# Kernel tuning notes

Measured on AMD Instinct MI355X. Metric: run time of the kernel, lower is better.

## Reference

```python
import jax, jax.numpy as jnp
import numpy as np

N = 100000
E = 800000
D = 128


def setup_inputs() -> dict:
    key = jax.random.key(0)
    k1, k2, k3, k4 = jax.random.split(key, 4)
    x = jax.random.normal(k1, (N, D), dtype=jnp.float32)
    edge_index = jax.random.randint(k2, (2, E), 0, N, dtype=jnp.int64)
    s = 1.0 / np.sqrt(D)
    W1 = jax.random.uniform(k3, (D, D), jnp.float32, -s, s)
    b1 = jnp.zeros((D,), jnp.float32)
    W2 = jax.random.uniform(k4, (D, D), jnp.float32, -s, s)
    b2 = jnp.zeros((D,), jnp.float32)
    return {"x": x, "edge_index": edge_index, "W1": W1, "b1": b1, "W2": W2, "b2": b2}


def _degree(idx, n, dtype):
    return jax.ops.segment_sum(jnp.ones(idx.shape, dtype), idx, num_segments=n)


def _graph_conv(x, row, col, W, b, residual, act):
    n = x.shape[0]
    deg_out = jnp.clip(_degree(row, n, x.dtype), 1.0)          # [N]
    x_src = x * jax.lax.rsqrt(deg_out)[:, None]                # [N, D]
    # scatter-add messages from source (row) into target (col)
    agg = jax.ops.segment_sum(x_src[row], col, num_segments=n)  # [N, D]
    out = agg @ W.T + b
    deg_in = jnp.clip(_degree(col, n, x.dtype), 1.0)
    out = out * jax.lax.rsqrt(deg_in)[:, None]
    if residual:
        out = out + x  # res_fc is Identity (in_dim == out_dim)
    if act:
        out = jax.nn.relu(out)
    return out


def reference(x, edge_index, W1, b1, W2, b2):
    row, col = edge_index[0], edge_index[1]
    # layer 1: relu + residual; layer 2 (last, encoding=False): no act, no residual
    h = _graph_conv(x, row, col, W1, b1, residual=True, act=True)
    h = _graph_conv(h, row, col, W2, b2, residual=False, act=False)
    return h
```

## Files before the change

kernel.cpp:

```cpp
#include <hip/hip_runtime.h>


#define NN 100000
#define EE 800000
#define DD 128
#define NB1 98
#define NTILE (NN / 16)

typedef __attribute__((ext_vector_type(8))) short short8;
typedef __attribute__((ext_vector_type(4))) float floatx4;

__device__ inline float bf2f(unsigned int u16) {
    union { unsigned int i; float f; } c;
    c.i = u16 << 16;
    return c.f;
}
__device__ inline ushort f2bf(float f) {
    union { float f; unsigned int i; } c;
    c.f = f;
    unsigned int u = c.i;
    return (ushort)((u + 0x7fffu + ((u >> 16) & 1u)) >> 16);
}

__global__ __launch_bounds__(256) void count_kernel(const int* __restrict__ row,
                                                    const int* __restrict__ col,
                                                    int* __restrict__ cnt_out,
                                                    int* __restrict__ cnt_in,
                                                    int* __restrict__ off) {
    int e = blockIdx.x * 256 + threadIdx.x;
    if (e < EE) {
        off[e] = atomicAdd(&cnt_in[col[e]], 1);
        atomicAdd(&cnt_out[row[e]], 1);
    }
}

__global__ __launch_bounds__(256) void dinv_kernel(const int* __restrict__ cnt_out,
                                                   const int* __restrict__ cnt_in,
                                                   float* __restrict__ dinv_out,
                                                   float* __restrict__ dinv_in) {
    int n = blockIdx.x * 256 + threadIdx.x;
    if (n < NN) {
        dinv_out[n] = rsqrtf((float)max(cnt_out[n], 1));
        dinv_in[n]  = rsqrtf((float)max(cnt_in[n], 1));
    }
}

__global__ __launch_bounds__(256) void scan1_kernel(const int* __restrict__ cnt,
                                                    int* __restrict__ excl,
                                                    int* __restrict__ bsums) {
    __shared__ int tmp[256];
    const int t = threadIdx.x;
    const int base = blockIdx.x * 1024 + t * 4;
    int a[4];
#pragma unroll
    for (int q = 0; q < 4; ++q) a[q] = (base + q < NN) ? cnt[base + q] : 0;
    int s = a[0] + a[1] + a[2] + a[3];
    tmp[t] = s;
    __syncthreads();
    for (int off = 1; off < 256; off <<= 1) {
        int v = 0;
        if (t >= off) v = tmp[t - off];
        __syncthreads();
        tmp[t] += v;
        __syncthreads();
    }
    int excl_s = tmp[t] - s;
    if (t == 255) bsums[blockIdx.x] = tmp[t];
    int run = excl_s;
#pragma unroll
    for (int q = 0; q < 4; ++q) {
        if (base + q < NN) excl[base + q] = run;
        run += a[q];
    }
}

__global__ __launch_bounds__(256) void scan2_kernel(int* __restrict__ bsums, int nb) {
    __shared__ int tmp[256];
    const int t = threadIdx.x;
    int s = (t < nb) ? bsums[t] : 0;
    tmp[t] = s;
    __syncthreads();
    for (int off = 1; off < 256; off <<= 1) {
        int v = 0;
        if (t >= off) v = tmp[t - off];
        __syncthreads();
        tmp[t] += v;
        __syncthreads();
    }
    if (t < nb) bsums[t] = tmp[t] - s;
}

__global__ __launch_bounds__(256) void scan3_kernel(const int* __restrict__ excl,
                                                    const int* __restrict__ bsums,
                                                    int* __restrict__ row_start) {
    int i = blockIdx.x * 256 + threadIdx.x;
    if (i < NN) row_start[i] = excl[i] + bsums[i >> 10];
}

__global__ __launch_bounds__(256) void fill_kernel(const int* __restrict__ row,
                                                   const int* __restrict__ col,
                                                   const int* __restrict__ row_start,
                                                   const int* __restrict__ off,
                                                   int* __restrict__ srcs) {
    int e = blockIdx.x * 256 + threadIdx.x;
    if (e < EE) srcs[row_start[col[e]] + off[e]] = row[e];
}

__global__ __launch_bounds__(256) void prescale_kernel(const float* __restrict__ x,
                                                       const float* __restrict__ dinv_out,
                                                       ushort* __restrict__ xb) {
    int idx = blockIdx.x * 256 + threadIdx.x;
    if (idx >= NN * 32) return;
    int n = idx >> 5;
    float s = dinv_out[n];
    float4 v = ((const float4*)x)[idx];
    ushort4 o;
    o.x = f2bf(v.x * s);
    o.y = f2bf(v.y * s);
    o.z = f2bf(v.z * s);
    o.w = f2bf(v.w * s);
    ((ushort4*)xb)[idx] = o;
}

__global__ __launch_bounds__(256) void gather_kernel(const ushort* __restrict__ src,
                                                     const int* __restrict__ row_start,
                                                     const int* __restrict__ srcs,
                                                     ushort* __restrict__ agg) {
    const int node = blockIdx.x * 16 + (threadIdx.x >> 4);
    const int lane = threadIdx.x & 15;
    if (node >= NN) return;
    int p = row_start[node];
    const int end = (node + 1 < NN) ? row_start[node + 1] : EE;
    float a0 = 0.f, a1 = 0.f, a2 = 0.f, a3 = 0.f;
    float a4 = 0.f, a5 = 0.f, a6 = 0.f, a7 = 0.f;

#define ACCUM(V)                                     \
    do {                                             \
        a0 += bf2f((V).x & 0xffffu);                 \
        a1 += bf2f((V).x >> 16);                     \
        a2 += bf2f((V).y & 0xffffu);                 \
        a3 += bf2f((V).y >> 16);                     \
        a4 += bf2f((V).z & 0xffffu);                 \
        a5 += bf2f((V).z >> 16);                     \
        a6 += bf2f((V).w & 0xffffu);                 \
        a7 += bf2f((V).w >> 16);                     \
    } while (0)

    for (; p + 3 < end; p += 4) {
        int s0 = srcs[p];
        int s1 = srcs[p + 1];
        int s2 = srcs[p + 2];
        int s3 = srcs[p + 3];
        uint4 v0 = ((const uint4*)(src + (size_t)s0 * DD))[lane];
        uint4 v1 = ((const uint4*)(src + (size_t)s1 * DD))[lane];
        uint4 v2 = ((const uint4*)(src + (size_t)s2 * DD))[lane];
        uint4 v3 = ((const uint4*)(src + (size_t)s3 * DD))[lane];
        ACCUM(v0); ACCUM(v1); ACCUM(v2); ACCUM(v3);
    }
    for (; p < end; ++p) {
        int s0 = srcs[p];
        uint4 v0 = ((const uint4*)(src + (size_t)s0 * DD))[lane];
        ACCUM(v0);
    }
#undef ACCUM

    uint4 o;
    o.x = (unsigned int)f2bf(a0) | ((unsigned int)f2bf(a1) << 16);
    o.y = (unsigned int)f2bf(a2) | ((unsigned int)f2bf(a3) << 16);
    o.z = (unsigned int)f2bf(a4) | ((unsigned int)f2bf(a5) << 16);
    o.w = (unsigned int)f2bf(a6) | ((unsigned int)f2bf(a7) << 16);
    ((uint4*)(agg + (size_t)node * DD))[lane] = o;
}

template <bool L1>
__global__ __launch_bounds__(256) void gemm_ep(const ushort* __restrict__ agg,
                                               const float* __restrict__ W,
                                               const float* __restrict__ bias,
                                               const float* __restrict__ dinv_in,
                                               const float* __restrict__ dinv_out,
                                               const float* __restrict__ x,
                                               ushort* __restrict__ hs,
                                               float* __restrict__ out) {
    __shared__ ushort Ws[128 * 136];
    {
        int j = threadIdx.x >> 1;
        int k0 = (threadIdx.x & 1) * 64;
        const float4* wp = (const float4*)(W + (size_t)j * DD + k0);
        ushort* dst = Ws + j * 136 + k0;
#pragma unroll
        for (int q = 0; q < 16; ++q) {
            float4 v = wp[q];
            ushort4 o;
            o.x = f2bf(v.x); o.y = f2bf(v.y); o.z = f2bf(v.z); o.w = f2bf(v.w);
            *(ushort4*)(dst + q * 4) = o;
        }
    }
    __syncthreads();

    const int wave = threadIdx.x >> 6;
    const int lane = threadIdx.x & 63;
    const int tile = blockIdx.x * 4 + wave;
    if (tile >= NTILE) return;
    const int mi = lane & 15;
    const int quad = lane >> 4;
    const int m0 = tile * 16;

    floatx4 acc[8];
#pragma unroll
    for (int t = 0; t < 8; ++t) acc[t] = (floatx4){0.f, 0.f, 0.f, 0.f};

    const ushort* ap = agg + (size_t)(m0 + mi) * DD + quad * 8;
#pragma unroll
    for (int s = 0; s < 4; ++s) {
        short8 a = *(const short8*)(ap + s * 32);
#pragma unroll
        for (int t = 0; t < 8; ++t) {
            short8 b = *(const short8*)(Ws + (t * 16 + mi) * 136 + s * 32 + quad * 8);
            acc[t] = __builtin_amdgcn_mfma_f32_16x16x32_bf16(a, b, acc[t], 0, 0, 0);
        }
    }

    float dv[4], dov[4];
#pragma unroll
    for (int i = 0; i < 4; ++i) {
        int r = m0 + quad * 4 + i;
        dv[i] = dinv_in[r];
        if (L1) dov[i] = dinv_out[r];
    }
#pragma unroll
    for (int t = 0; t < 8; ++t) {
        int c = t * 16 + mi;
        float bv = bias[c];
#pragma unroll
        for (int i = 0; i < 4; ++i) {
            int r = m0 + quad * 4 + i;
            float o = (acc[t][i] + bv) * dv[i];
            if (L1) {
                o += x[(size_t)r * DD + c];
                o = fmaxf(o, 0.f);
                hs[(size_t)r * DD + c] = f2bf(o * dov[i]);
            } else {
                out[(size_t)r * DD + c] = o;
            }
        }
    }
}

extern "C" void kernel_launch(void* const* d_in, const int* in_sizes, int n_in,
                              void* d_out, int out_size, void* d_ws, size_t ws_size,
                              hipStream_t stream) {
    const float* x  = (const float*)d_in[0];
    const int*   ei = (const int*)d_in[1];
    const float* W1 = (const float*)d_in[2];
    const float* b1 = (const float*)d_in[3];
    const float* W2 = (const float*)d_in[4];
    const float* b2 = (const float*)d_in[5];
    float* out = (float*)d_out;

    const int* row = ei;
    const int* col = ei + EE;

    ushort* agg     = (ushort*)d_ws;
    ushort* xb      = agg + (size_t)NN * DD;
    float* dinv_out = (float*)(xb + (size_t)NN * DD);
    float* dinv_in  = dinv_out + NN;
    int*   cnt      = (int*)(dinv_in + NN);
    int*   excl     = cnt + 2 * NN;
    int*   row_st   = excl + NN;
    int*   srcs     = row_st + NN;
    int*   bsums    = srcs + EE;
    int*   off      = (int*)agg;

    hipMemsetAsync(cnt, 0, 2 * NN * sizeof(int), stream);
    count_kernel<<<(EE + 255) / 256, 256, 0, stream>>>(row, col, cnt, cnt + NN, off);
    dinv_kernel<<<(NN + 255) / 256, 256, 0, stream>>>(cnt, cnt + NN, dinv_out, dinv_in);
    scan1_kernel<<<NB1, 256, 0, stream>>>(cnt + NN, excl, bsums);
    scan2_kernel<<<1, 256, 0, stream>>>(bsums, NB1);
    scan3_kernel<<<(NN + 255) / 256, 256, 0, stream>>>(excl, bsums, row_st);
    fill_kernel<<<(EE + 255) / 256, 256, 0, stream>>>(row, col, row_st, off, srcs);

    prescale_kernel<<<(NN * 32 + 255) / 256, 256, 0, stream>>>(x, dinv_out, xb);
    gather_kernel<<<(NN + 15) / 16, 256, 0, stream>>>(xb, row_st, srcs, agg);
    gemm_ep<true><<<(NTILE + 3) / 4, 256, 0, stream>>>(agg, W1, b1, dinv_in, dinv_out, x,
                                                       xb, nullptr);

    gather_kernel<<<(NN + 15) / 16, 256, 0, stream>>>(xb, row_st, srcs, agg);
    gemm_ep<false><<<(NTILE + 3) / 4, 256, 0, stream>>>(agg, W2, b2, dinv_in, nullptr, nullptr,
                                                        nullptr, out);
}
```

Baseline: 321.2 us.

## Privatize degree counters per XCD with workgroup-scope atomics

```diff
diff --git a/kernel.cpp b/kernel.cpp
--- a/kernel.cpp
+++ b/kernel.cpp
@@ -6,6 +6,7 @@
 #define DD 128
 #define NB1 98
 #define NTILE (NN / 16)
+#define NXCD 8
 
 typedef __attribute__((ext_vector_type(8))) short short8;
 typedef __attribute__((ext_vector_type(4))) float floatx4;
@@ -22,27 +23,48 @@
     return (ushort)((u + 0x7fffu + ((u >> 16) & 1u)) >> 16);
 }
 
+__device__ inline unsigned int xcc_id() {
+    unsigned int x;
+    asm volatile("s_getreg_b32 %0, hwreg(HW_REG_XCC_ID)" : "=s"(x));
+    return x & (NXCD - 1);
+}
+
 __global__ __launch_bounds__(256) void count_kernel(const int* __restrict__ row,
                                                     const int* __restrict__ col,
-                                                    int* __restrict__ cnt_out,
-                                                    int* __restrict__ cnt_in,
+                                                    int* __restrict__ partial_out,
+                                                    int* __restrict__ partial_in,
                                                     int* __restrict__ off) {
     int e = blockIdx.x * 256 + threadIdx.x;
     if (e < EE) {
-        off[e] = atomicAdd(&cnt_in[col[e]], 1);
-        atomicAdd(&cnt_out[row[e]], 1);
-    }
-}
-
-__global__ __launch_bounds__(256) void dinv_kernel(const int* __restrict__ cnt_out,
-                                                   const int* __restrict__ cnt_in,
+        unsigned int k = xcc_id();
+        int c = col[e];
+        int slot = __hip_atomic_fetch_add(&partial_in[k * NN + c], 1,
+                                          __ATOMIC_RELAXED, __HIP_MEMORY_SCOPE_WORKGROUP);
+        off[e] = slot | (int)(k << 28);
+        __hip_atomic_fetch_add(&partial_out[k * NN + row[e]], 1,
+                               __ATOMIC_RELAXED, __HIP_MEMORY_SCOPE_WORKGROUP);
+    }
+}
+
+__global__ __launch_bounds__(256) void node_kernel(const int* __restrict__ partial_out,
+                                                   const int* __restrict__ partial_in,
+                                                   int* __restrict__ cnt_total,
+                                                   int* __restrict__ xoff,
                                                    float* __restrict__ dinv_out,
                                                    float* __restrict__ dinv_in) {
     int n = blockIdx.x * 256 + threadIdx.x;
-    if (n < NN) {
-        dinv_out[n] = rsqrtf((float)max(cnt_out[n], 1));
-        dinv_in[n]  = rsqrtf((float)max(cnt_in[n], 1));
-    }
+    if (n >= NN) return;
+    int din = 0, dout = 0;
+#pragma unroll
+    for (int k = 0; k < NXCD; ++k) {
+        int v = partial_in[k * NN + n];
+        xoff[k * NN + n] = din;
+        din += v;
+        dout += partial_out[k * NN + n];
+    }
+    cnt_total[n] = din;
+    dinv_in[n]  = rsqrtf((float)max(din, 1));
+    dinv_out[n] = rsqrtf((float)max(dout, 1));
 }
 
 __global__ __launch_bounds__(256) void scan1_kernel(const int* __restrict__ cnt,
@@ -100,10 +122,17 @@
 __global__ __launch_bounds__(256) void fill_kernel(const int* __restrict__ row,
                                                    const int* __restrict__ col,
                                                    const int* __restrict__ row_start,
+                                                   const int* __restrict__ xoff,
                                                    const int* __restrict__ off,
                                                    int* __restrict__ srcs) {
     int e = blockIdx.x * 256 + threadIdx.x;
-    if (e < EE) srcs[row_start[col[e]] + off[e]] = row[e];
+    if (e < EE) {
+        int c = col[e];
+        unsigned int o = (unsigned int)off[e];
+        int k = (int)(o >> 28);
+        int slot = (int)(o & 0x0FFFFFFFu);
+        srcs[row_start[c] + xoff[k * NN + c] + slot] = row[e];
+    }
 }
 
 __global__ __launch_bounds__(256) void prescale_kernel(const float* __restrict__ x,
@@ -269,15 +298,20 @@
     int*   row_st   = excl + NN;
     int*   srcs     = row_st + NN;
     int*   bsums    = srcs + EE;
-    int*   off      = (int*)agg;
-
-    hipMemsetAsync(cnt, 0, 2 * NN * sizeof(int), stream);
-    count_kernel<<<(EE + 255) / 256, 256, 0, stream>>>(row, col, cnt, cnt + NN, off);
-    dinv_kernel<<<(NN + 255) / 256, 256, 0, stream>>>(cnt, cnt + NN, dinv_out, dinv_in);
-    scan1_kernel<<<NB1, 256, 0, stream>>>(cnt + NN, excl, bsums);
+
+    int* off         = (int*)agg;
+    int* partial_in  = off + EE;
+    int* partial_out = partial_in + NXCD * NN;
+    int* xoff        = partial_out + NXCD * NN;
+
+    hipMemsetAsync(partial_in, 0, (size_t)2 * NXCD * NN * sizeof(int), stream);
+    count_kernel<<<(EE + 255) / 256, 256, 0, stream>>>(row, col, partial_out, partial_in, off);
+    node_kernel<<<(NN + 255) / 256, 256, 0, stream>>>(partial_out, partial_in, cnt, xoff,
+                                                      dinv_out, dinv_in);
+    scan1_kernel<<<NB1, 256, 0, stream>>>(cnt, excl, bsums);
     scan2_kernel<<<1, 256, 0, stream>>>(bsums, NB1);
     scan3_kernel<<<(NN + 255) / 256, 256, 0, stream>>>(excl, bsums, row_st);
-    fill_kernel<<<(EE + 255) / 256, 256, 0, stream>>>(row, col, row_st, off, srcs);
+    fill_kernel<<<(EE + 255) / 256, 256, 0, stream>>>(row, col, row_st, xoff, off, srcs);
 
     prescale_kernel<<<(NN * 32 + 255) / 256, 256, 0, stream>>>(x, dinv_out, xb);
     gather_kernel<<<(NN + 15) / 16, 256, 0, stream>>>(xb, row_st, srcs, agg);
```

After: 319.6 us. No clear change (-0.5%).

## Replace global atomic degree counting with chunked LDS byte-packed histograms

Applied to the files above, without the earlier changes.

```diff
diff --git a/kernel.cpp b/kernel.cpp
--- a/kernel.cpp
+++ b/kernel.cpp
@@ -7,6 +7,12 @@
 #define NB1 98
 #define NTILE (NN / 16)
 
+#define CC 64
+#define CH (EE / CC)
+#define HALF 50000
+#define HWORDS 12500
+#define NWORDS 25000
+
 typedef __attribute__((ext_vector_type(8))) short short8;
 typedef __attribute__((ext_vector_type(4))) float floatx4;
 
@@ -22,27 +28,67 @@
     return (ushort)((u + 0x7fffu + ((u >> 16) & 1u)) >> 16);
 }
 
-__global__ __launch_bounds__(256) void count_kernel(const int* __restrict__ row,
+__global__ __launch_bounds__(512) void count_kernel(const int* __restrict__ row,
                                                     const int* __restrict__ col,
-                                                    int* __restrict__ cnt_out,
-                                                    int* __restrict__ cnt_in,
-                                                    int* __restrict__ off) {
-    int e = blockIdx.x * 256 + threadIdx.x;
-    if (e < EE) {
-        off[e] = atomicAdd(&cnt_in[col[e]], 1);
-        atomicAdd(&cnt_out[row[e]], 1);
-    }
-}
-
-__global__ __launch_bounds__(256) void dinv_kernel(const int* __restrict__ cnt_out,
-                                                   const int* __restrict__ cnt_in,
+                                                    unsigned int* __restrict__ partial_out,
+                                                    unsigned int* __restrict__ partial_in,
+                                                    unsigned char* __restrict__ off_u8) {
+    __shared__ unsigned int h[HWORDS];
+    for (int i = threadIdx.x; i < HWORDS; i += 512) h[i] = 0;
+    __syncthreads();
+
+    const int kind = blockIdx.x >> 7;
+    const int r = (blockIdx.x >> 6) & 1;
+    const int c = blockIdx.x & 63;
+    const int* __restrict__ idx = kind ? row : col;
+    const int base = c * CH;
+    const int lo = r * HALF;
+
+    for (int t = threadIdx.x; t < CH; t += 512) {
+        const int e = base + t;
+        const unsigned int d = (unsigned int)(idx[e] - lo);
+        if (d < (unsigned int)HALF) {
+            const int sh = 8 * (d & 3);
+            unsigned int old = atomicAdd(&h[d >> 2], 1u << sh);
+            if (kind == 0) off_u8[e] = (unsigned char)((old >> sh) & 0xffu);
+        }
+    }
+    __syncthreads();
+
+    unsigned int* dst = (kind ? partial_out : partial_in) + c * NWORDS + r * HWORDS;
+    for (int i = threadIdx.x; i < HWORDS; i += 512) dst[i] = h[i];
+}
+
+__global__ __launch_bounds__(256) void node_kernel(const unsigned int* __restrict__ partial_out,
+                                                   const unsigned int* __restrict__ partial_in,
+                                                   int* __restrict__ cnt_total,
+                                                   unsigned int* __restrict__ xoff,
                                                    float* __restrict__ dinv_out,
                                                    float* __restrict__ dinv_in) {
-    int n = blockIdx.x * 256 + threadIdx.x;
-    if (n < NN) {
-        dinv_out[n] = rsqrtf((float)max(cnt_out[n], 1));
-        dinv_in[n]  = rsqrtf((float)max(cnt_in[n], 1));
-    }
+    const int w = blockIdx.x * 256 + threadIdx.x;
+    if (w >= NWORDS) return;
+    unsigned int prefix = 0;
+    unsigned int tot_out = 0;
+#pragma unroll
+    for (int c = 0; c < CC; ++c) {
+        unsigned int v = partial_in[c * NWORDS + w];
+        xoff[c * NWORDS + w] = prefix;
+        prefix += v;
+        tot_out += partial_out[c * NWORDS + w];
+    }
+    int4 ct;
+    float4 fi, fo;
+#pragma unroll
+    for (int j = 0; j < 4; ++j) {
+        int din  = (int)((prefix  >> (8 * j)) & 0xffu);
+        int dout = (int)((tot_out >> (8 * j)) & 0xffu);
+        ((int*)&ct)[j]   = din;
+        ((float*)&fi)[j] = rsqrtf((float)max(din, 1));
+        ((float*)&fo)[j] = rsqrtf((float)max(dout, 1));
+    }
+    ((int4*)cnt_total)[w] = ct;
+    ((float4*)dinv_in)[w] = fi;
+    ((float4*)dinv_out)[w] = fo;
 }
 
 __global__ __launch_bounds__(256) void scan1_kernel(const int* __restrict__ cnt,
@@ -100,10 +146,16 @@
 __global__ __launch_bounds__(256) void fill_kernel(const int* __restrict__ row,
                                                    const int* __restrict__ col,
                                                    const int* __restrict__ row_start,
-                                                   const int* __restrict__ off,
+                                                   const unsigned char* __restrict__ xoff_u8,
+                                                   const unsigned char* __restrict__ off_u8,
                                                    int* __restrict__ srcs) {
     int e = blockIdx.x * 256 + threadIdx.x;
-    if (e < EE) srcs[row_start[col[e]] + off[e]] = row[e];
+    if (e < EE) {
+        const int cl = col[e];
+        const int c = e / CH;
+        const int pos = row_start[cl] + (int)xoff_u8[(size_t)c * NN + cl] + (int)off_u8[e];
+        srcs[pos] = row[e];
+    }
 }
 
 __global__ __launch_bounds__(256) void prescale_kernel(const float* __restrict__ x,
@@ -265,19 +317,24 @@
     float* dinv_out = (float*)(xb + (size_t)NN * DD);
     float* dinv_in  = dinv_out + NN;
     int*   cnt      = (int*)(dinv_in + NN);
-    int*   excl     = cnt + 2 * NN;
+    int*   excl     = cnt + NN;
     int*   row_st   = excl + NN;
     int*   srcs     = row_st + NN;
     int*   bsums    = srcs + EE;
-    int*   off      = (int*)agg;
-
-    hipMemsetAsync(cnt, 0, 2 * NN * sizeof(int), stream);
-    count_kernel<<<(EE + 255) / 256, 256, 0, stream>>>(row, col, cnt, cnt + NN, off);
-    dinv_kernel<<<(NN + 255) / 256, 256, 0, stream>>>(cnt, cnt + NN, dinv_out, dinv_in);
-    scan1_kernel<<<NB1, 256, 0, stream>>>(cnt + NN, excl, bsums);
+
+    unsigned char* off_u8      = (unsigned char*)agg;
+    unsigned int*  partial_in  = (unsigned int*)(off_u8 + EE);
+    unsigned int*  partial_out = partial_in + CC * NWORDS;
+    unsigned int*  xoff        = partial_out + CC * NWORDS;
+
+    count_kernel<<<256, 512, 0, stream>>>(row, col, partial_out, partial_in, off_u8);
+    node_kernel<<<(NWORDS + 255) / 256, 256, 0, stream>>>(partial_out, partial_in, cnt, xoff,
+                                                          dinv_out, dinv_in);
+    scan1_kernel<<<NB1, 256, 0, stream>>>(cnt, excl, bsums);
     scan2_kernel<<<1, 256, 0, stream>>>(bsums, NB1);
     scan3_kernel<<<(NN + 255) / 256, 256, 0, stream>>>(excl, bsums, row_st);
-    fill_kernel<<<(EE + 255) / 256, 256, 0, stream>>>(row, col, row_st, off, srcs);
+    fill_kernel<<<(EE + 255) / 256, 256, 0, stream>>>(row, col, row_st,
+                                                      (const unsigned char*)xoff, off_u8, srcs);
 
     prescale_kernel<<<(NN * 32 + 255) / 256, 256, 0, stream>>>(x, dinv_out, xb);
     gather_kernel<<<(NN + 15) / 16, 256, 0, stream>>>(xb, row_st, srcs, agg);
```

New measurement: 280.9 us. -12.6%, faster.
